# Kernel optimization log

Measured on AMD Instinct MI355X. Metric: run time of the kernel, lower is better.

## Reference

```python
import jax, jax.numpy as jnp
import numpy as np

D = 128       # d_model
NHEAD = 4
R = 2         # n_rounds
CF = 32       # fine channels
H0, W0 = 40, 52
HF, WF = 160, 208
TEMP = 0.1
THR = 0.2
WIN = 5
STRIDE = 8


def setup_inputs() -> dict:
    key = jax.random.key(0)
    ks = jax.random.split(key, 24)
    s = 0.05
    f = jnp.float32
    n = lambda k, sh: jax.random.normal(k, sh, f)
    inp = {
        'coarse0': n(ks[0], (1, D, H0, W0)),
        'coarse1': n(ks[1], (1, D, H0, W0)),
        'fine0': n(ks[2], (1, CF, HF, WF)),
        'fine1': n(ks[3], (1, CF, HF, WF)),
        'sa_in_w': n(ks[4], (R, 3 * D, D)) * s,
        'sa_in_b': jnp.zeros((R, 3 * D), f),
        'sa_out_w': n(ks[5], (R, D, D)) * s,
        'sa_out_b': jnp.zeros((R, D), f),
        'ca_in_w': n(ks[6], (R, 3 * D, D)) * s,
        'ca_in_b': jnp.zeros((R, 3 * D), f),
        'ca_out_w': n(ks[7], (R, D, D)) * s,
        'ca_out_b': jnp.zeros((R, D), f),
        'sn_g': jnp.ones((R, D), f), 'sn_b': jnp.zeros((R, D), f),
        'cn_g': jnp.ones((R, D), f), 'cn_b': jnp.zeros((R, D), f),
        'ffn_w1': n(ks[8], (R, 2 * D, D)) * s,
        'ffn_b1': jnp.zeros((R, 2 * D), f),
        'ffn_w2': n(ks[9], (R, D, 2 * D)) * s,
        'ffn_b2': jnp.zeros((R, D), f),
        'fn_g': jnp.ones((R, D), f), 'fn_b': jnp.zeros((R, D), f),
        'proj_w': n(ks[10], (CF, CF)) * s,
        'proj_b': jnp.zeros((CF,), f),
    }
    return inp


def _ln(x, g, b):
    m = x.mean(-1, keepdims=True)
    v = ((x - m) ** 2).mean(-1, keepdims=True)
    return (x - m) * jax.lax.rsqrt(v + 1e-5) * g + b


def _mha(xq, xkv, in_w, in_b, out_w, out_b):
    B, Lq, d = xq.shape
    Lk = xkv.shape[1]
    h, dh = NHEAD, D // NHEAD
    q = (xq @ in_w[:d].T + in_b[:d]).reshape(B, Lq, h, dh)
    k = (xkv @ in_w[d:2 * d].T + in_b[d:2 * d]).reshape(B, Lk, h, dh)
    v = (xkv @ in_w[2 * d:].T + in_b[2 * d:]).reshape(B, Lk, h, dh)
    a = jnp.einsum('bqhd,bkhd->bhqk', q, k) / np.float32(np.sqrt(dh))
    a = jax.nn.softmax(a, axis=-1)
    o = jnp.einsum('bhqk,bkhd->bqhd', a, v).reshape(B, Lq, d)
    return o @ out_w.T + out_b


def _forward(coarse0, coarse1, fine0, fine1, sa_in_w, sa_in_b, sa_out_w, sa_out_b,
             ca_in_w, ca_in_b, ca_out_w, ca_out_b, sn_g, sn_b, cn_g, cn_b,
             ffn_w1, ffn_b1, ffn_w2, ffn_b2, fn_g, fn_b, proj_w, proj_b):
    B, C, H, W = coarse0.shape
    f0 = coarse0.reshape(B, C, H * W).transpose(0, 2, 1)
    f1 = coarse1.reshape(B, C, H * W).transpose(0, 2, 1)
    for i in range(R):
        f0 = _ln(f0 + _mha(f0, f0, sa_in_w[i], sa_in_b[i], sa_out_w[i], sa_out_b[i]), sn_g[i], sn_b[i])
        f1 = _ln(f1 + _mha(f1, f1, sa_in_w[i], sa_in_b[i], sa_out_w[i], sa_out_b[i]), sn_g[i], sn_b[i])
        f0c = _mha(f0, f1, ca_in_w[i], ca_in_b[i], ca_out_w[i], ca_out_b[i])
        f1c = _mha(f1, f0, ca_in_w[i], ca_in_b[i], ca_out_w[i], ca_out_b[i])
        f0 = _ln(f0 + f0c, cn_g[i], cn_b[i])
        f1 = _ln(f1 + f1c, cn_g[i], cn_b[i])
        f0 = _ln(f0 + jax.nn.relu(f0 @ ffn_w1[i].T + ffn_b1[i]) @ ffn_w2[i].T + ffn_b2[i], fn_g[i], fn_b[i])
        f1 = _ln(f1 + jax.nn.relu(f1 @ ffn_w1[i].T + ffn_b1[i]) @ ffn_w2[i].T + ffn_b2[i], fn_g[i], fn_b[i])
    # coarse matching: dual softmax + mutual NN
    f0n = f0 / jnp.maximum(jnp.linalg.norm(f0, axis=-1, keepdims=True), 1e-12)
    f1n = f1 / jnp.maximum(jnp.linalg.norm(f1, axis=-1, keepdims=True), 1e-12)
    S = jnp.einsum('bld,bmd->blm', f0n, f1n) / TEMP
    P = jax.nn.softmax(S, axis=-1) * jax.nn.softmax(S, axis=-2)
    P0 = P[0]
    L0 = H * W
    idx0 = jnp.argmax(P0, axis=-1)
    idx1 = jnp.argmax(P0, axis=0)
    conf = P0.max(axis=-1)
    valid = (idx1[idx0] == jnp.arange(L0)) & (conf > THR)
    ar = jnp.arange(L0)
    mk0 = jnp.stack([ar % W, ar // W], 1).astype(jnp.float32)
    mk1 = jnp.stack([idx0 % W, idx0 // W], 1).astype(jnp.float32)
    # fine refinement (vectorized over all L0 candidate matches)
    f0p = jnp.einsum('oc,chw->ohw', proj_w, fine0[0]) + proj_b[:, None, None]
    f1p = jnp.einsum('oc,chw->ohw', proj_w, fine1[0]) + proj_b[:, None, None]
    half = WIN // 2
    fr = STRIDE // 2
    c0 = (mk0 * fr).astype(jnp.int32)
    c1 = (mk1 * fr).astype(jnp.int32)
    Hf, Wf = f0p.shape[1], f0p.shape[2]
    inb = ((c0[:, 0] - half >= 0) & (c0[:, 0] + half < Wf) & (c0[:, 1] - half >= 0) & (c0[:, 1] + half < Hf)
           & (c1[:, 0] - half >= 0) & (c1[:, 0] + half < Wf) & (c1[:, 1] - half >= 0) & (c1[:, 1] + half < Hf))
    off = jnp.arange(WIN) - half
    cy0 = jnp.clip(c0[:, 1], half, Hf - 1 - half)
    cx0 = jnp.clip(c0[:, 0], half, Wf - 1 - half)
    cy1 = jnp.clip(c1[:, 1], half, Hf - 1 - half)
    cx1 = jnp.clip(c1[:, 0], half, Wf - 1 - half)
    center = f0p[:, cy0, cx0]                              # (C, N)
    y1 = cy1[:, None] + off
    x1 = cx1[:, None] + off
    patch1 = f1p[:, y1[:, :, None], x1[:, None, :]]
    corr = jnp.einsum('cn,cnhw->nhw', center, patch1)
    soft = jax.nn.softmax(corr.reshape(-1, WIN * WIN), axis=-1).reshape(-1, WIN, WIN)
    gx = off.astype(jnp.float32)[None, None, :]
    gy = off.astype(jnp.float32)[None, :, None]
    offx = (soft * gx).sum((1, 2))
    offy = (soft * gy).sum((1, 2))
    scale = np.float32(STRIDE // fr)
    pt0 = mk0 * STRIDE + STRIDE // 2
    base1 = mk1 * STRIDE + STRIDE // 2
    delta = jnp.stack([offx, offy], 1) * scale
    pt1 = base1 + jnp.where(inb[:, None], delta, 0.0)
    return P, valid, conf, pt0, pt1


def reference(coarse0, coarse1, fine0, fine1, sa_in_w, sa_in_b, sa_out_w, sa_out_b,
              ca_in_w, ca_in_b, ca_out_w, ca_out_b, sn_g, sn_b, cn_g, cn_b,
              ffn_w1, ffn_b1, ffn_w2, ffn_b2, fn_g, fn_b, proj_w, proj_b):
    return _forward(coarse0, coarse1, fine0, fine1, sa_in_w, sa_in_b, sa_out_w, sa_out_b,
                    ca_in_w, ca_in_b, ca_out_w, ca_out_b, sn_g, sn_b, cn_g, cn_b,
                    ffn_w1, ffn_b1, ffn_w2, ffn_b2, fn_g, fn_b, proj_w, proj_b)
```

## Files before the change

kernel.cpp:

```cpp
#include <hip/hip_runtime.h>
#include <math.h>

#define LTOK 2080
#define DIM 128
#define NH 4
#define W0C 52
#define HFI 160
#define WFI 208
#define NPIX (HFI*WFI)
#define CFCH 32
#define NSPLIT 5
#define PARTSTRIDE 1056

__global__ __launch_bounds__(256) void transpose_b_kernel(const float* __restrict__ in0,
                                                          const float* __restrict__ in1,
                                                          float* __restrict__ out0,
                                                          float* __restrict__ out1)
{
    const float* in = blockIdx.z ? in1 : in0;
    float* out = blockIdx.z ? out1 : out0;
    __shared__ float T[32][33];
    int l0 = blockIdx.x * 32, c0 = blockIdx.y * 32;
    int t = threadIdx.x;
    #pragma unroll
    for (int e = 0; e < 4; ++e) {
        int idx = t + e * 256; int i = idx >> 5, j = idx & 31;
        T[i][j] = in[(size_t)(c0 + i) * LTOK + l0 + j];
    }
    __syncthreads();
    #pragma unroll
    for (int e = 0; e < 4; ++e) {
        int idx = t + e * 256; int j2 = idx >> 5, i2 = idx & 31;
        out[(size_t)(l0 + j2) * DIM + c0 + i2] = T[i2][j2];
    }
}

__global__ __launch_bounds__(256) void gemm_nt_b2_kernel(const float* __restrict__ A0,
                                                         const float* __restrict__ A1, int lda,
                                                         const float* __restrict__ B, int ldb,
                                                         float* __restrict__ C0,
                                                         float* __restrict__ C1, int ldc,
                                                         int K,
                                                         const float* __restrict__ bias, int relu)
{
    const float* A = blockIdx.z ? A1 : A0;
    float* C = blockIdx.z ? C1 : C0;
    __shared__ float As[32][33];
    __shared__ float Bs[32][33];
    int tid = threadIdx.x;
    int n0 = blockIdx.x * 32, m0 = blockIdx.y * 32;
    int c = tid & 31, r8 = tid >> 5;
    float acc[4] = {0.f, 0.f, 0.f, 0.f};
    for (int k0 = 0; k0 < K; k0 += 32) {
        #pragma unroll
        for (int e = 0; e < 4; ++e) {
            int l = tid + e * 256;
            int i = l >> 5, k = l & 31;
            As[k][i] = A[(size_t)(m0 + i) * lda + k0 + k];
            Bs[k][i] = B[(size_t)(n0 + i) * ldb + k0 + k];
        }
        __syncthreads();
        #pragma unroll
        for (int k = 0; k < 32; ++k) {
            float bv = Bs[k][c];
            #pragma unroll
            for (int jj = 0; jj < 4; ++jj)
                acc[jj] += As[k][4 * r8 + jj] * bv;
        }
        __syncthreads();
    }
    #pragma unroll
    for (int jj = 0; jj < 4; ++jj) {
        float v = acc[jj];
        if (bias) v += bias[n0 + c];
        if (relu) v = fmaxf(v, 0.f);
        C[(size_t)(m0 + 4 * r8 + jj) * ldc + n0 + c] = v;
    }
}

__global__ __launch_bounds__(256) void gemm_score_kernel(const float* __restrict__ A,
                                                         const float* __restrict__ B,
                                                         float* __restrict__ C,
                                                         float2* __restrict__ prs,
                                                         float2* __restrict__ pcs)
{
    __shared__ float As[32][33];
    __shared__ float Bs[32][33];
    __shared__ float cmS[8][32];
    __shared__ float ceS[8][32];
    int tid = threadIdx.x;
    int n0 = blockIdx.x * 32, m0 = blockIdx.y * 32;
    int c = tid & 31, r8 = tid >> 5;
    float acc[4] = {0.f, 0.f, 0.f, 0.f};
    for (int k0 = 0; k0 < 128; k0 += 32) {
        #pragma unroll
        for (int e = 0; e < 4; ++e) {
            int l = tid + e * 256;
            int i = l >> 5, k = l & 31;
            As[k][i] = A[(size_t)(m0 + i) * 128 + k0 + k];
            Bs[k][i] = B[(size_t)(n0 + i) * 128 + k0 + k];
        }
        __syncthreads();
        #pragma unroll
        for (int k = 0; k < 32; ++k) {
            float bv = Bs[k][c];
            #pragma unroll
            for (int jj = 0; jj < 4; ++jj)
                acc[jj] += As[k][4 * r8 + jj] * bv;
        }
        __syncthreads();
    }
    float v[4];
    #pragma unroll
    for (int jj = 0; jj < 4; ++jj) {
        v[jj] = 10.f * acc[jj];
        C[(size_t)(m0 + 4 * r8 + jj) * LTOK + n0 + c] = v[jj];
    }
    #pragma unroll
    for (int jj = 0; jj < 4; ++jj) {
        float m = v[jj];
        #pragma unroll
        for (int mm = 16; mm >= 1; mm >>= 1) m = fmaxf(m, __shfl_xor(m, mm, 32));
        float e = __expf(v[jj] - m);
        #pragma unroll
        for (int mm = 16; mm >= 1; mm >>= 1) e += __shfl_xor(e, mm, 32);
        if (c == 0) prs[(size_t)blockIdx.x * LTOK + m0 + 4 * r8 + jj] = make_float2(m, e);
    }
    float cmx = fmaxf(fmaxf(v[0], v[1]), fmaxf(v[2], v[3]));
    float cex = __expf(v[0] - cmx) + __expf(v[1] - cmx) + __expf(v[2] - cmx) + __expf(v[3] - cmx);
    cmS[r8][c] = cmx; ceS[r8][c] = cex;
    __syncthreads();
    if (r8 == 0) {
        float M = cmS[0][c], S = ceS[0][c];
        #pragma unroll
        for (int k = 1; k < 8; ++k) {
            float m2 = cmS[k][c], s2 = ceS[k][c];
            if (m2 > M) { S = S * __expf(M - m2) + s2; M = m2; }
            else        { S += s2 * __expf(m2 - M); }
        }
        pcs[(size_t)blockIdx.y * LTOK + n0 + c] = make_float2(M, S);
    }
}

__global__ __launch_bounds__(256) void stats_combine_kernel(const float2* __restrict__ prs,
                                                            const float2* __restrict__ pcs,
                                                            float* __restrict__ rowmax,
                                                            float* __restrict__ rsinv,
                                                            float* __restrict__ colmax,
                                                            float* __restrict__ csinv)
{
    int id = blockIdx.x * 256 + threadIdx.x;
    if (id >= 2 * LTOK) return;
    const float2* p = (id < LTOK) ? (prs + id) : (pcs + (id - LTOK));
    float M = -1e30f;
    for (int i = 0; i < 65; ++i) M = fmaxf(M, p[(size_t)i * LTOK].x);
    float S = 0.f;
    for (int i = 0; i < 65; ++i) {
        float2 f = p[(size_t)i * LTOK];
        S += f.y * __expf(f.x - M);
    }
    if (id < LTOK) { rowmax[id] = M; rsinv[id] = 1.f / S; }
    else           { colmax[id - LTOK] = M; csinv[id - LTOK] = 1.f / S; }
}

__global__ __launch_bounds__(256) void dualp_argmax_kernel(float* __restrict__ S,
                                                           const float* __restrict__ rm,
                                                           const float* __restrict__ rsinv,
                                                           const float* __restrict__ cm,
                                                           const float* __restrict__ csinv,
                                                           float* __restrict__ prv,
                                                           int* __restrict__ pri,
                                                           float* __restrict__ pcv,
                                                           int* __restrict__ pci)
{
    __shared__ float cvS[8][32];
    __shared__ int   ciS[8][32];
    int tid = threadIdx.x;
    int n0 = blockIdx.x * 32, m0 = blockIdx.y * 32;
    int c = tid & 31, r8 = tid >> 5;
    int col = n0 + c;
    float cmv = cm[col], csv = csinv[col];
    float p[4];
    #pragma unroll
    for (int jj = 0; jj < 4; ++jj) {
        int row = m0 + 4 * r8 + jj;
        size_t o = (size_t)row * LTOK + col;
        float s = S[o];
        float pv = __expf(2.f * s - rm[row] - cmv) * (rsinv[row] * csv);
        S[o] = pv;
        p[jj] = pv;
    }
    #pragma unroll
    for (int jj = 0; jj < 4; ++jj) {
        float bv = p[jj]; int bi = col;
        #pragma unroll
        for (int mm = 16; mm >= 1; mm >>= 1) {
            float ov = __shfl_xor(bv, mm, 32);
            int   oi = __shfl_xor(bi, mm, 32);
            if (ov > bv || (ov == bv && oi < bi)) { bv = ov; bi = oi; }
        }
        if (c == 0) {
            prv[(size_t)blockIdx.x * LTOK + m0 + 4 * r8 + jj] = bv;
            pri[(size_t)blockIdx.x * LTOK + m0 + 4 * r8 + jj] = bi;
        }
    }
    float bv = p[0]; int bi = m0 + 4 * r8;
    #pragma unroll
    for (int jj = 1; jj < 4; ++jj)
        if (p[jj] > bv) { bv = p[jj]; bi = m0 + 4 * r8 + jj; }
    cvS[r8][c] = bv; ciS[r8][c] = bi;
    __syncthreads();
    if (r8 == 0) {
        #pragma unroll
        for (int k = 1; k < 8; ++k)
            if (cvS[k][c] > bv) { bv = cvS[k][c]; bi = ciS[k][c]; }
        pcv[(size_t)blockIdx.y * LTOK + col] = bv;
        pci[(size_t)blockIdx.y * LTOK + col] = bi;
    }
}

__global__ __launch_bounds__(256) void argmax_combine_kernel(const float* __restrict__ prv,
                                                             const int* __restrict__ pri,
                                                             const float* __restrict__ pcv,
                                                             const int* __restrict__ pci,
                                                             int* __restrict__ idx0,
                                                             float* __restrict__ conf,
                                                             int* __restrict__ idx1)
{
    int id = blockIdx.x * 256 + threadIdx.x;
    if (id >= 2 * LTOK) return;
    if (id < LTOK) {
        float best = -1e30f; int bi = 0;
        for (int i = 0; i < 65; ++i) {
            float v = prv[(size_t)i * LTOK + id];
            if (v > best) { best = v; bi = pri[(size_t)i * LTOK + id]; }
        }
        idx0[id] = bi; conf[id] = best;
    } else {
        int colI = id - LTOK;
        float best = -1e30f; int bi = 0;
        for (int i = 0; i < 65; ++i) {
            float v = pcv[(size_t)i * LTOK + colI];
            if (v > best) { best = v; bi = pci[(size_t)i * LTOK + colI]; }
        }
        idx1[colI] = bi;
    }
}

__global__ __launch_bounds__(256, 4) void mha_partial_b_kernel(const float* __restrict__ qkvA,
                                                               const float* __restrict__ qkvB,
                                                               int cross,
                                                               float* __restrict__ part)
{
    __shared__ float Qs[32][36];
    __shared__ float Ks[64][36];
    __shared__ float Vt[32][68];
    __shared__ float Ps[32][68];
    int tid = threadIdx.x;
    int qb = blockIdx.x, ns = blockIdx.z;
    int img = blockIdx.y >> 2, h = blockIdx.y & 3;
    const float* qsrc  = img ? qkvB : qkvA;
    const float* kvsrc = cross ? (img ? qkvA : qkvB) : qsrc;
    int c = tid & 31, r8 = tid >> 5;
    int row0 = 4 * r8;
    const float sc = 0.17677669529663687f;

    {
        int r = tid >> 3, d4 = (tid & 7) << 2;
        float4 q = *(const float4*)(qsrc + (size_t)(qb * 32 + r) * 384 + h * 32 + d4);
        *(float4*)(&Qs[r][d4]) = q;
    }
    float acc[4] = {0.f, 0.f, 0.f, 0.f};
    float lacc[4] = {0.f, 0.f, 0.f, 0.f};
    __syncthreads();

    const int koff = 128 + h * 32, voff = 256 + h * 32;
    for (int t = ns; t < 33; t += NSPLIT) {
        int j0 = t * 64;
        {
            int r = tid >> 3, d4 = (tid & 7) << 2;
            int j1 = j0 + r, j2 = j0 + r + 32;
            float4 k1 = *(const float4*)(kvsrc + (size_t)j1 * 384 + koff + d4);
            float4 v1 = *(const float4*)(kvsrc + (size_t)j1 * 384 + voff + d4);
            float4 k2 = make_float4(0.f, 0.f, 0.f, 0.f);
            float4 v2 = make_float4(0.f, 0.f, 0.f, 0.f);
            if (j2 < LTOK) {
                k2 = *(const float4*)(kvsrc + (size_t)j2 * 384 + koff + d4);
                v2 = *(const float4*)(kvsrc + (size_t)j2 * 384 + voff + d4);
            }
            *(float4*)(&Ks[r][d4])      = k1;
            *(float4*)(&Ks[r + 32][d4]) = k2;
            Vt[d4 + 0][r] = v1.x; Vt[d4 + 1][r] = v1.y; Vt[d4 + 2][r] = v1.z; Vt[d4 + 3][r] = v1.w;
            Vt[d4 + 0][r + 32] = v2.x; Vt[d4 + 1][r + 32] = v2.y; Vt[d4 + 2][r + 32] = v2.z; Vt[d4 + 3][r + 32] = v2.w;
        }
        __syncthreads();
        float s1[4] = {0.f, 0.f, 0.f, 0.f};
        float s2[4] = {0.f, 0.f, 0.f, 0.f};
        #pragma unroll
        for (int d4 = 0; d4 < 8; ++d4) {
            float4 ka = *(const float4*)(&Ks[c][d4 << 2]);
            float4 kb = *(const float4*)(&Ks[c + 32][d4 << 2]);
            #pragma unroll
            for (int jj = 0; jj < 4; ++jj) {
                float4 q = *(const float4*)(&Qs[row0 + jj][d4 << 2]);
                s1[jj] += q.x * ka.x + q.y * ka.y + q.z * ka.z + q.w * ka.w;
                s2[jj] += q.x * kb.x + q.y * kb.y + q.z * kb.z + q.w * kb.w;
            }
        }
        bool ok2 = (j0 + 32 + c) < LTOK;
        #pragma unroll
        for (int jj = 0; jj < 4; ++jj) {
            float p1 = __expf(s1[jj] * sc);
            float p2 = ok2 ? __expf(s2[jj] * sc) : 0.f;
            Ps[row0 + jj][c] = p1;
            Ps[row0 + jj][c + 32] = p2;
            lacc[jj] += p1 + p2;
        }
        __syncthreads();
        #pragma unroll
        for (int j4 = 0; j4 < 16; ++j4) {
            float4 vv = *(const float4*)(&Vt[c][j4 << 2]);
            #pragma unroll
            for (int jj = 0; jj < 4; ++jj) {
                float4 pp = *(const float4*)(&Ps[row0 + jj][j4 << 2]);
                acc[jj] += pp.x * vv.x + pp.y * vv.y + pp.z * vv.z + pp.w * vv.w;
            }
        }
        __syncthreads();
    }
    float* pb = part + (size_t)((((size_t)img * 65 + qb) * NH + h) * NSPLIT + ns) * PARTSTRIDE;
    #pragma unroll
    for (int jj = 0; jj < 4; ++jj)
        pb[(row0 + jj) * 32 + c] = acc[jj];
    #pragma unroll
    for (int jj = 0; jj < 4; ++jj) {
        float l = lacc[jj];
        #pragma unroll
        for (int mm = 16; mm >= 1; mm >>= 1) l += __shfl_xor(l, mm, 32);
        if (c == 0) pb[1024 + row0 + jj] = l;
    }
}

__global__ __launch_bounds__(256) void mha_combine_b_kernel(const float* __restrict__ part,
                                                            float* __restrict__ out0,
                                                            float* __restrict__ out1)
{
    int tid = threadIdx.x;
    int qb = blockIdx.x;
    int img = blockIdx.y >> 2, h = blockIdx.y & 3;
    float* out = img ? out1 : out0;
    int c = tid & 31, r8 = tid >> 5;
    int row0 = 4 * r8;
    const float* pb = part + (size_t)(((size_t)img * 65 + qb) * NH + h) * NSPLIT * PARTSTRIDE;
    #pragma unroll
    for (int jj = 0; jj < 4; ++jj) {
        int row = row0 + jj;
        float num = 0.f, den = 0.f;
        #pragma unroll
        for (int ns = 0; ns < NSPLIT; ++ns) {
            num += pb[ns * PARTSTRIDE + row * 32 + c];
            den += pb[ns * PARTSTRIDE + 1024 + row];
        }
        out[(size_t)(qb * 32 + row) * DIM + h * 32 + c] = num / den;
    }
}

__global__ __launch_bounds__(256) void addln_b_kernel(float* __restrict__ f0,
                                                      float* __restrict__ f1,
                                                      const float* __restrict__ t0,
                                                      const float* __restrict__ t1,
                                                      const float* __restrict__ g,
                                                      const float* __restrict__ b)
{
    float* f = blockIdx.y ? f1 : f0;
    const float* t = blockIdx.y ? t1 : t0;
    int row = blockIdx.x * 4 + (threadIdx.x >> 6);
    int lane = threadIdx.x & 63;
    size_t base = (size_t)row * DIM;
    float x0 = f[base + lane] + t[base + lane];
    float x1 = f[base + lane + 64] + t[base + lane + 64];
    float s = x0 + x1;
    #pragma unroll
    for (int mm = 32; mm >= 1; mm >>= 1) s += __shfl_xor(s, mm, 64);
    float mean = s * (1.f / 128.f);
    float d0 = x0 - mean, d1 = x1 - mean;
    float v = d0 * d0 + d1 * d1;
    #pragma unroll
    for (int mm = 32; mm >= 1; mm >>= 1) v += __shfl_xor(v, mm, 64);
    float rstd = rsqrtf(v * (1.f / 128.f) + 1e-5f);
    f[base + lane]      = d0 * rstd * g[lane] + b[lane];
    f[base + lane + 64] = d1 * rstd * g[lane + 64] + b[lane + 64];
}

__global__ __launch_bounds__(256) void normrows_b_kernel(const float* __restrict__ i0,
                                                         const float* __restrict__ i1,
                                                         float* __restrict__ o0,
                                                         float* __restrict__ o1)
{
    const float* f = blockIdx.y ? i1 : i0;
    float* o = blockIdx.y ? o1 : o0;
    int row = blockIdx.x * 4 + (threadIdx.x >> 6);
    int lane = threadIdx.x & 63;
    size_t base = (size_t)row * DIM;
    float x0 = f[base + lane], x1 = f[base + lane + 64];
    float v = x0 * x0 + x1 * x1;
    #pragma unroll
    for (int mm = 32; mm >= 1; mm >>= 1) v += __shfl_xor(v, mm, 64);
    float inv = 1.f / fmaxf(sqrtf(v), 1e-12f);
    o[base + lane] = x0 * inv;
    o[base + lane + 64] = x1 * inv;
}

__global__ __launch_bounds__(256) void match_kernel(const int* __restrict__ idx0,
                                                    const int* __restrict__ idx1,
                                                    const float* __restrict__ conf,
                                                    float* __restrict__ out_valid,
                                                    float* __restrict__ out_conf,
                                                    float* __restrict__ out_pt0)
{
    int i = blockIdx.x * 256 + threadIdx.x;
    if (i >= LTOK) return;
    int j = idx0[i];
    bool valid = (idx1[j] == i) && (conf[i] > 0.2f);
    out_valid[i] = valid ? 1.f : 0.f;
    out_conf[i] = conf[i];
    out_pt0[2 * i]     = (float)(i % W0C) * 8.f + 4.f;
    out_pt0[2 * i + 1] = (float)(i / W0C) * 8.f + 4.f;
}

__global__ __launch_bounds__(256) void fine_proj_b_kernel(const float* __restrict__ fin0,
                                                          const float* __restrict__ fin1,
                                                          const float* __restrict__ w,
                                                          const float* __restrict__ b,
                                                          float* __restrict__ fout0,
                                                          float* __restrict__ fout1)
{
    const float* fin = blockIdx.y ? fin1 : fin0;
    float* fout = blockIdx.y ? fout1 : fout0;
    __shared__ float ws_[32][32];
    __shared__ float bs[32];
    int t = threadIdx.x;
    #pragma unroll
    for (int e = 0; e < 4; ++e) { int l = t + e * 256; ws_[l >> 5][l & 31] = w[l]; }
    if (t < 32) bs[t] = b[t];
    __syncthreads();
    int p = blockIdx.x * 256 + t;
    if (p >= NPIX) return;
    float x[32];
    #pragma unroll
    for (int cc = 0; cc < 32; ++cc) x[cc] = fin[(size_t)cc * NPIX + p];
    #pragma unroll
    for (int o = 0; o < 32; ++o) {
        float a = bs[o];
        #pragma unroll
        for (int cc = 0; cc < 32; ++cc) a += ws_[o][cc] * x[cc];
        fout[(size_t)o * NPIX + p] = a;
    }
}

__global__ __launch_bounds__(64) void fine_match_kernel(const int* __restrict__ idx0,
                                                        const float* __restrict__ f0p,
                                                        const float* __restrict__ f1p,
                                                        float* __restrict__ out_pt1)
{
    int i = blockIdx.x;
    int l = threadIdx.x;
    int j = idx0[i];
    int m0x = i % W0C, m0y = i / W0C;
    int m1x = j % W0C, m1y = j / W0C;
    int c0x = m0x * 4, c0y = m0y * 4, c1x = m1x * 4, c1y = m1y * 4;
    bool inb = (c0x - 2 >= 0) && (c0x + 2 < WFI) && (c0y - 2 >= 0) && (c0y + 2 < HFI)
            && (c1x - 2 >= 0) && (c1x + 2 < WFI) && (c1y - 2 >= 0) && (c1y + 2 < HFI);
    int cy0 = min(max(c0y, 2), HFI - 3), cx0 = min(max(c0x, 2), WFI - 3);
    int cy1 = min(max(c1y, 2), HFI - 3), cx1 = min(max(c1x, 2), WFI - 3);
    int dy = l / 5 - 2, dx = l % 5 - 2;
    float corr = -1e30f;
    if (l < 25) {
        float a = 0.f;
        int p0 = cy0 * WFI + cx0;
        int p1 = (cy1 + dy) * WFI + (cx1 + dx);
        #pragma unroll
        for (int cc = 0; cc < 32; ++cc)
            a += f0p[(size_t)cc * NPIX + p0] * f1p[(size_t)cc * NPIX + p1];
        corr = a;
    }
    float mx = corr;
    #pragma unroll
    for (int mm = 32; mm >= 1; mm >>= 1) mx = fmaxf(mx, __shfl_xor(mx, mm, 64));
    float p = (l < 25) ? expf(corr - mx) : 0.f;
    float s = p, sx = p * (float)dx, sy = p * (float)dy;
    #pragma unroll
    for (int mm = 32; mm >= 1; mm >>= 1) {
        s  += __shfl_xor(s, mm, 64);
        sx += __shfl_xor(sx, mm, 64);
        sy += __shfl_xor(sy, mm, 64);
    }
    if (l == 0) {
        float offx = sx / s, offy = sy / s;
        float px = (float)m1x * 8.f + 4.f;
        float py = (float)m1y * 8.f + 4.f;
        if (inb) { px += offx * 2.f; py += offy * 2.f; }
        out_pt1[2 * i]     = px;
        out_pt1[2 * i + 1] = py;
    }
}

extern "C" void kernel_launch(void* const* d_in, const int* in_sizes, int n_in,
                              void* d_out, int out_size, void* d_ws, size_t ws_size,
                              hipStream_t stream) {
    (void)in_sizes; (void)n_in; (void)out_size; (void)ws_size;
    const float* coarse0 = (const float*)d_in[0];
    const float* coarse1 = (const float*)d_in[1];
    const float* fine0   = (const float*)d_in[2];
    const float* fine1   = (const float*)d_in[3];
    const float* sa_in_w  = (const float*)d_in[4];
    const float* sa_in_b  = (const float*)d_in[5];
    const float* sa_out_w = (const float*)d_in[6];
    const float* sa_out_b = (const float*)d_in[7];
    const float* ca_in_w  = (const float*)d_in[8];
    const float* ca_in_b  = (const float*)d_in[9];
    const float* ca_out_w = (const float*)d_in[10];
    const float* ca_out_b = (const float*)d_in[11];
    const float* sn_g = (const float*)d_in[12];
    const float* sn_b = (const float*)d_in[13];
    const float* cn_g = (const float*)d_in[14];
    const float* cn_b = (const float*)d_in[15];
    const float* ffn_w1 = (const float*)d_in[16];
    const float* ffn_b1 = (const float*)d_in[17];
    const float* ffn_w2 = (const float*)d_in[18];
    const float* ffn_b2 = (const float*)d_in[19];
    const float* fn_g = (const float*)d_in[20];
    const float* fn_b = (const float*)d_in[21];
    const float* proj_w = (const float*)d_in[22];
    const float* proj_b = (const float*)d_in[23];

    float* w = (float*)d_ws;
    float* f0   = w; w += (size_t)LTOK * DIM;
    float* f1   = w; w += (size_t)LTOK * DIM;
    float* qkv0 = w; w += (size_t)LTOK * 384;
    float* qkv1 = w; w += (size_t)LTOK * 384;
    float* att0 = w; w += (size_t)LTOK * DIM;
    float* att1 = w; w += (size_t)LTOK * DIM;
    float* tmp0 = w; w += (size_t)LTOK * DIM;
    float* tmp1 = w; w += (size_t)LTOK * DIM;
    float* f0n  = w; w += (size_t)LTOK * DIM;
    float* f1n  = w; w += (size_t)LTOK * DIM;
    float* R1   = w; w += (size_t)2 * 65 * NH * NSPLIT * PARTSTRIDE;
    float* rowmax = w; w += LTOK;
    float* rsinv  = w; w += LTOK;
    float* colmax = w; w += LTOK;
    float* csinv  = w; w += LTOK;
    float* conf   = w; w += LTOK;
    int* idx0 = (int*)w; w += LTOK;
    int* idx1 = (int*)w; w += LTOK;

    float* part = R1;
    float* hid0 = R1;
    float* hid1 = R1 + (size_t)LTOK * 256;
    float* f0p  = R1;
    float* f1p  = R1 + (size_t)CFCH * NPIX;

    float2* prs = (float2*)qkv0;
    float2* pcs = (float2*)(qkv0 + 2 * 65 * LTOK);
    float*  prv = qkv1;
    int*    pri = (int*)(qkv1 + 65 * LTOK);
    float*  pcv = qkv1 + 2 * 65 * LTOK;
    int*    pci = (int*)(qkv1 + 3 * 65 * LTOK);

    float* Pout = (float*)d_out;
    float* out_valid = Pout + (size_t)LTOK * LTOK;
    float* out_conf  = out_valid + LTOK;
    float* out_pt0   = out_conf + LTOK;
    float* out_pt1   = out_pt0 + 2 * LTOK;

    dim3 b256(256);
    dim3 gMHA(65, 8, NSPLIT);
    dim3 gCMB(65, 8);
    dim3 gLN(520, 2);
    transpose_b_kernel<<<dim3(65, 4, 2), b256, 0, stream>>>(coarse0, coarse1, f0, f1);

    for (int i = 0; i < 2; ++i) {
        const float* saw = sa_in_w + (size_t)i * 384 * 128;
        const float* sab = sa_in_b + (size_t)i * 384;
        const float* sow = sa_out_w + (size_t)i * 128 * 128;
        const float* sob = sa_out_b + (size_t)i * 128;
        const float* caw = ca_in_w + (size_t)i * 384 * 128;
        const float* cab = ca_in_b + (size_t)i * 384;
        const float* cow = ca_out_w + (size_t)i * 128 * 128;
        const float* cob = ca_out_b + (size_t)i * 128;
        const float* w1 = ffn_w1 + (size_t)i * 256 * 128;
        const float* b1 = ffn_b1 + (size_t)i * 256;
        const float* w2 = ffn_w2 + (size_t)i * 128 * 256;
        const float* b2 = ffn_b2 + (size_t)i * 128;

        gemm_nt_b2_kernel<<<dim3(12, 65, 2), b256, 0, stream>>>(f0, f1, 128, saw, 128, qkv0, qkv1, 384, 128, sab, 0);
        mha_partial_b_kernel<<<gMHA, b256, 0, stream>>>(qkv0, qkv1, 0, part);
        mha_combine_b_kernel<<<gCMB, b256, 0, stream>>>(part, att0, att1);
        gemm_nt_b2_kernel<<<dim3(4, 65, 2), b256, 0, stream>>>(att0, att1, 128, sow, 128, tmp0, tmp1, 128, 128, sob, 0);
        addln_b_kernel<<<gLN, b256, 0, stream>>>(f0, f1, tmp0, tmp1, sn_g + (size_t)i * 128, sn_b + (size_t)i * 128);

        gemm_nt_b2_kernel<<<dim3(12, 65, 2), b256, 0, stream>>>(f0, f1, 128, caw, 128, qkv0, qkv1, 384, 128, cab, 0);
        mha_partial_b_kernel<<<gMHA, b256, 0, stream>>>(qkv0, qkv1, 1, part);
        mha_combine_b_kernel<<<gCMB, b256, 0, stream>>>(part, att0, att1);
        gemm_nt_b2_kernel<<<dim3(4, 65, 2), b256, 0, stream>>>(att0, att1, 128, cow, 128, tmp0, tmp1, 128, 128, cob, 0);
        addln_b_kernel<<<gLN, b256, 0, stream>>>(f0, f1, tmp0, tmp1, cn_g + (size_t)i * 128, cn_b + (size_t)i * 128);

        gemm_nt_b2_kernel<<<dim3(8, 65, 2), b256, 0, stream>>>(f0, f1, 128, w1, 128, hid0, hid1, 256, 128, b1, 1);
        gemm_nt_b2_kernel<<<dim3(4, 65, 2), b256, 0, stream>>>(hid0, hid1, 256, w2, 256, tmp0, tmp1, 128, 256, b2, 0);
        addln_b_kernel<<<gLN, b256, 0, stream>>>(f0, f1, tmp0, tmp1, fn_g + (size_t)i * 128, fn_b + (size_t)i * 128);
    }

    normrows_b_kernel<<<gLN, b256, 0, stream>>>(f0, f1, f0n, f1n);
    gemm_score_kernel<<<dim3(65, 65), b256, 0, stream>>>(f0n, f1n, Pout, prs, pcs);
    stats_combine_kernel<<<17, b256, 0, stream>>>(prs, pcs, rowmax, rsinv, colmax, csinv);
    dualp_argmax_kernel<<<dim3(65, 65), b256, 0, stream>>>(Pout, rowmax, rsinv, colmax, csinv,
                                                           prv, pri, pcv, pci);
    argmax_combine_kernel<<<17, b256, 0, stream>>>(prv, pri, pcv, pci, idx0, conf, idx1);
    match_kernel<<<9, b256, 0, stream>>>(idx0, idx1, conf, out_valid, out_conf, out_pt0);

    fine_proj_b_kernel<<<dim3(130, 2), b256, 0, stream>>>(fine0, fine1, proj_w, proj_b, f0p, f1p);
    fine_match_kernel<<<LTOK, dim3(64), 0, stream>>>(idx0, f0p, f1p, out_pt1);
}
```

Baseline: 919.0 us.

## Enlarge attention query tile to 64 rows and cut KV split count

After: 3.576 ms. 3.89x slower.

```diff
diff --git a/kernel.cpp b/kernel.cpp
--- a/kernel.cpp
+++ b/kernel.cpp
@@ -9,8 +9,10 @@
 #define WFI 208
 #define NPIX (HFI*WFI)
 #define CFCH 32
-#define NSPLIT 5
-#define PARTSTRIDE 1056
+#define NSPLIT2 3
+#define QBLK 64
+#define NQB 33
+#define PSTRIDE2 2112
 
 __global__ __launch_bounds__(256) void transpose_b_kernel(const float* __restrict__ in0,
                                                           const float* __restrict__ in1,
@@ -247,35 +249,37 @@
     }
 }
 
-__global__ __launch_bounds__(256, 4) void mha_partial_b_kernel(const float* __restrict__ qkvA,
-                                                               const float* __restrict__ qkvB,
-                                                               int cross,
-                                                               float* __restrict__ part)
-{
-    __shared__ float Qs[32][36];
+__global__ __launch_bounds__(256, 3) void mha_partial2_kernel(const float* __restrict__ qkvA,
+                                                              const float* __restrict__ qkvB,
+                                                              int cross,
+                                                              float* __restrict__ part)
+{
+    __shared__ float Qs[QBLK][36];
     __shared__ float Ks[64][36];
     __shared__ float Vt[32][68];
-    __shared__ float Ps[32][68];
+    __shared__ float Ps[QBLK][68];
     int tid = threadIdx.x;
     int qb = blockIdx.x, ns = blockIdx.z;
     int img = blockIdx.y >> 2, h = blockIdx.y & 3;
     const float* qsrc  = img ? qkvB : qkvA;
     const float* kvsrc = cross ? (img ? qkvA : qkvB) : qsrc;
-    int c = tid & 31, r8 = tid >> 5;
-    int row0 = 4 * r8;
+    int c4 = tid & 15;
+    int rg = tid >> 4;
     const float sc = 0.17677669529663687f;
 
     {
-        int r = tid >> 3, d4 = (tid & 7) << 2;
-        float4 q = *(const float4*)(qsrc + (size_t)(qb * 32 + r) * 384 + h * 32 + d4);
-        *(float4*)(&Qs[r][d4]) = q;
-    }
-    float acc[4] = {0.f, 0.f, 0.f, 0.f};
+        int r = tid >> 2, d8 = (tid & 3) << 3;
+        int qr = qb * QBLK + r; qr = qr < LTOK ? qr : (LTOK - 1);
+        const float* src = qsrc + (size_t)qr * 384 + h * 32 + d8;
+        *(float4*)(&Qs[r][d8])     = *(const float4*)(src);
+        *(float4*)(&Qs[r][d8 + 4]) = *(const float4*)(src + 4);
+    }
+    float acc[4][2] = {{0.f,0.f},{0.f,0.f},{0.f,0.f},{0.f,0.f}};
     float lacc[4] = {0.f, 0.f, 0.f, 0.f};
     __syncthreads();
 
     const int koff = 128 + h * 32, voff = 256 + h * 32;
-    for (int t = ns; t < 33; t += NSPLIT) {
+    for (int t = ns; t < 33; t += NSPLIT2) {
         int j0 = t * 64;
         {
             int r = tid >> 3, d4 = (tid & 7) << 2;
@@ -294,74 +298,87 @@
             Vt[d4 + 0][r + 32] = v2.x; Vt[d4 + 1][r + 32] = v2.y; Vt[d4 + 2][r + 32] = v2.z; Vt[d4 + 3][r + 32] = v2.w;
         }
         __syncthreads();
-        float s1[4] = {0.f, 0.f, 0.f, 0.f};
-        float s2[4] = {0.f, 0.f, 0.f, 0.f};
+        float s[4][4] = {{0.f,0.f,0.f,0.f},{0.f,0.f,0.f,0.f},{0.f,0.f,0.f,0.f},{0.f,0.f,0.f,0.f}};
         #pragma unroll
         for (int d4 = 0; d4 < 8; ++d4) {
-            float4 ka = *(const float4*)(&Ks[c][d4 << 2]);
-            float4 kb = *(const float4*)(&Ks[c + 32][d4 << 2]);
+            float4 kf[4];
+            #pragma unroll
+            for (int k = 0; k < 4; ++k) kf[k] = *(const float4*)(&Ks[k * 16 + c4][d4 << 2]);
             #pragma unroll
             for (int jj = 0; jj < 4; ++jj) {
-                float4 q = *(const float4*)(&Qs[row0 + jj][d4 << 2]);
-                s1[jj] += q.x * ka.x + q.y * ka.y + q.z * ka.z + q.w * ka.w;
-                s2[jj] += q.x * kb.x + q.y * kb.y + q.z * kb.z + q.w * kb.w;
+                float4 q = *(const float4*)(&Qs[rg * 4 + jj][d4 << 2]);
+                #pragma unroll
+                for (int k = 0; k < 4; ++k)
+                    s[jj][k] += q.x * kf[k].x + q.y * kf[k].y + q.z * kf[k].z + q.w * kf[k].w;
             }
         }
-        bool ok2 = (j0 + 32 + c) < LTOK;
         #pragma unroll
         for (int jj = 0; jj < 4; ++jj) {
-            float p1 = __expf(s1[jj] * sc);
-            float p2 = ok2 ? __expf(s2[jj] * sc) : 0.f;
-            Ps[row0 + jj][c] = p1;
-            Ps[row0 + jj][c + 32] = p2;
-            lacc[jj] += p1 + p2;
+            float4 pv;
+            float* pp = (float*)&pv;
+            #pragma unroll
+            for (int k = 0; k < 4; ++k) {
+                bool ok = (j0 + k * 16 + c4) < LTOK;
+                pp[k] = ok ? __expf(s[jj][k] * sc) : 0.f;
+                lacc[jj] += pp[k];
+            }
+            Ps[rg * 4 + jj][c4]      = pv.x;
+            Ps[rg * 4 + jj][c4 + 16] = pv.y;
+            Ps[rg * 4 + jj][c4 + 32] = pv.z;
+            Ps[rg * 4 + jj][c4 + 48] = pv.w;
         }
         __syncthreads();
         #pragma unroll
         for (int j4 = 0; j4 < 16; ++j4) {
-            float4 vv = *(const float4*)(&Vt[c][j4 << 2]);
+            float4 v0 = *(const float4*)(&Vt[c4][j4 << 2]);
+            float4 v1 = *(const float4*)(&Vt[c4 + 16][j4 << 2]);
             #pragma unroll
             for (int jj = 0; jj < 4; ++jj) {
-                float4 pp = *(const float4*)(&Ps[row0 + jj][j4 << 2]);
-                acc[jj] += pp.x * vv.x + pp.y * vv.y + pp.z * vv.z + pp.w * vv.w;
+                float4 pq = *(const float4*)(&Ps[rg * 4 + jj][j4 << 2]);
+                acc[jj][0] += pq.x * v0.x + pq.y * v0.y + pq.z * v0.z + pq.w * v0.w;
+                acc[jj][1] += pq.x * v1.x + pq.y * v1.y + pq.z * v1.z + pq.w * v1.w;
             }
         }
         __syncthreads();
     }
-    float* pb = part + (size_t)((((size_t)img * 65 + qb) * NH + h) * NSPLIT + ns) * PARTSTRIDE;
-    #pragma unroll
-    for (int jj = 0; jj < 4; ++jj)
-        pb[(row0 + jj) * 32 + c] = acc[jj];
+    float* pb = part + (size_t)((((size_t)img * NQB + qb) * NH + h) * NSPLIT2 + ns) * PSTRIDE2;
+    #pragma unroll
+    for (int jj = 0; jj < 4; ++jj) {
+        int row = rg * 4 + jj;
+        pb[row * 32 + c4]      = acc[jj][0];
+        pb[row * 32 + c4 + 16] = acc[jj][1];
+    }
     #pragma unroll
     for (int jj = 0; jj < 4; ++jj) {
         float l = lacc[jj];
         #pragma unroll
-        for (int mm = 16; mm >= 1; mm >>= 1) l += __shfl_xor(l, mm, 32);
-        if (c == 0) pb[1024 + row0 + jj] = l;
-    }
-}
-
-__global__ __launch_bounds__(256) void mha_combine_b_kernel(const float* __restrict__ part,
-                                                            float* __restrict__ out0,
-                                                            float* __restrict__ out1)
+        for (int mm = 8; mm >= 1; mm >>= 1) l += __shfl_xor(l, mm, 16);
+        if (c4 == 0) pb[2048 + rg * 4 + jj] = l;
+    }
+}
+
+__global__ __launch_bounds__(256) void mha_combine2_kernel(const float* __restrict__ part,
+                                                           float* __restrict__ out0,
+                                                           float* __restrict__ out1)
 {
     int tid = threadIdx.x;
     int qb = blockIdx.x;
     int img = blockIdx.y >> 2, h = blockIdx.y & 3;
     float* out = img ? out1 : out0;
-    int c = tid & 31, r8 = tid >> 5;
-    int row0 = 4 * r8;
-    const float* pb = part + (size_t)(((size_t)img * 65 + qb) * NH + h) * NSPLIT * PARTSTRIDE;
-    #pragma unroll
-    for (int jj = 0; jj < 4; ++jj) {
-        int row = row0 + jj;
+    int c = tid & 31, rg8 = tid >> 5;
+    const float* pb = part + (size_t)(((size_t)img * NQB + qb) * NH + h) * NSPLIT2 * PSTRIDE2;
+    #pragma unroll
+    for (int jj = 0; jj < 8; ++jj) {
+        int row = rg8 * 8 + jj;
+        int qrow = qb * QBLK + row;
+        if (qrow >= LTOK) continue;
         float num = 0.f, den = 0.f;
         #pragma unroll
-        for (int ns = 0; ns < NSPLIT; ++ns) {
-            num += pb[ns * PARTSTRIDE + row * 32 + c];
-            den += pb[ns * PARTSTRIDE + 1024 + row];
-        }
-        out[(size_t)(qb * 32 + row) * DIM + h * 32 + c] = num / den;
+        for (int ns = 0; ns < NSPLIT2; ++ns) {
+            num += pb[ns * PSTRIDE2 + row * 32 + c];
+            den += pb[ns * PSTRIDE2 + 2048 + row];
+        }
+        out[(size_t)qrow * DIM + h * 32 + c] = num / den;
     }
 }
 
@@ -545,7 +562,7 @@
     float* tmp1 = w; w += (size_t)LTOK * DIM;
     float* f0n  = w; w += (size_t)LTOK * DIM;
     float* f1n  = w; w += (size_t)LTOK * DIM;
-    float* R1   = w; w += (size_t)2 * 65 * NH * NSPLIT * PARTSTRIDE;
+    float* R1   = w; w += (size_t)2745600;
     float* rowmax = w; w += LTOK;
     float* rsinv  = w; w += LTOK;
     float* colmax = w; w += LTOK;
@@ -574,8 +591,8 @@
     float* out_pt1   = out_pt0 + 2 * LTOK;
 
     dim3 b256(256);
-    dim3 gMHA(65, 8, NSPLIT);
-    dim3 gCMB(65, 8);
+    dim3 gMHA(NQB, 8, NSPLIT2);
+    dim3 gCMB(NQB, 8);
     dim3 gLN(520, 2);
     transpose_b_kernel<<<dim3(65, 4, 2), b256, 0, stream>>>(coarse0, coarse1, f0, f1);
 
@@ -594,14 +611,14 @@
         const float* b2 = ffn_b2 + (size_t)i * 128;
 
         gemm_nt_b2_kernel<<<dim3(12, 65, 2), b256, 0, stream>>>(f0, f1, 128, saw, 128, qkv0, qkv1, 384, 128, sab, 0);
-        mha_partial_b_kernel<<<gMHA, b256, 0, stream>>>(qkv0, qkv1, 0, part);
-        mha_combine_b_kernel<<<gCMB, b256, 0, stream>>>(part, att0, att1);
+        mha_partial2_kernel<<<gMHA, b256, 0, stream>>>(qkv0, qkv1, 0, part);
+        mha_combine2_kernel<<<gCMB, b256, 0, stream>>>(part, att0, att1);
         gemm_nt_b2_kernel<<<dim3(4, 65, 2), b256, 0, stream>>>(att0, att1, 128, sow, 128, tmp0, tmp1, 128, 128, sob, 0);
         addln_b_kernel<<<gLN, b256, 0, stream>>>(f0, f1, tmp0, tmp1, sn_g + (size_t)i * 128, sn_b + (size_t)i * 128);
 
         gemm_nt_b2_kernel<<<dim3(12, 65, 2), b256, 0, stream>>>(f0, f1, 128, caw, 128, qkv0, qkv1, 384, 128, cab, 0);
-        mha_partial_b_kernel<<<gMHA, b256, 0, stream>>>(qkv0, qkv1, 1, part);
-        mha_combine_b_kernel<<<gCMB, b256, 0, stream>>>(part, att0, att1);
+        mha_partial2_kernel<<<gMHA, b256, 0, stream>>>(qkv0, qkv1, 1, part);
+        mha_combine2_kernel<<<gCMB, b256, 0, stream>>>(part, att0, att1);
         gemm_nt_b2_kernel<<<dim3(4, 65, 2), b256, 0, stream>>>(att0, att1, 128, cow, 128, tmp0, tmp1, 128, 128, cob, 0);
         addln_b_kernel<<<gLN, b256, 0, stream>>>(f0, f1, tmp0, tmp1, cn_g + (size_t)i * 128, cn_b + (size_t)i * 128);
 
```
